# Kernel optimization log

Hardware: AMD Instinct MI355X
Metric: run time of the kernel (lower is better)

The kernel has to match this reference:

```python
import jax, jax.numpy as jnp
import numpy as np

N, T, F, H = 20000, 64, 32, 64
E = 640000
G1, G2 = 64, 32


def _lstm_layer(x_seq, Wih, Whh, bih, bhh):
    # x_seq: [N, T, Fin] -> hs [N, T, H], PyTorch gate order i,f,g,o
    n, _, _ = x_seq.shape
    h_dim = Whh.shape[1]
    h0 = jnp.zeros((n, h_dim), x_seq.dtype)
    c0 = jnp.zeros((n, h_dim), x_seq.dtype)

    def step(carry, xt):
        h, c = carry
        gates = xt @ Wih.T + h @ Whh.T + bih + bhh
        i, f, g, o = jnp.split(gates, 4, axis=-1)
        c = jax.nn.sigmoid(f) * c + jax.nn.sigmoid(i) * jnp.tanh(g)
        h = jax.nn.sigmoid(o) * jnp.tanh(c)
        return (h, c), h

    (_, _), hs = jax.lax.scan(step, (h0, c0), jnp.swapaxes(x_seq, 0, 1))
    return jnp.swapaxes(hs, 0, 1)


def _gcn(h, src, dst, W, b):
    # GCNConv (PyG default): add self-loops, symmetric deg^-1/2 normalization
    n = h.shape[0]
    loop = jnp.arange(n)
    s = jnp.concatenate([src, loop])
    d = jnp.concatenate([dst, loop])
    deg = jax.ops.segment_sum(jnp.ones_like(d, dtype=h.dtype), d, num_segments=n)
    dinv = jnp.where(deg > 0, deg ** -0.5, 0.0)
    norm = dinv[s] * dinv[d]
    xw = h @ W                      # [n, out]
    msg = xw[s] * norm[:, None]     # gather on source nodes
    return jax.ops.segment_sum(msg, d, num_segments=n) + b


def setup_inputs() -> dict:
    key = jax.random.key(0)
    ks = jax.random.split(key, 16)
    s = 0.1
    inp = {
        "x": jax.random.normal(ks[0], (N, T, F), jnp.float32),
        "stock_ids": jax.random.randint(ks[1], (N,), 0, N),
        "edge_index": jax.random.randint(ks[2], (2, E), 0, N),
        # LSTM layer 0
        "Wih0": jax.random.normal(ks[3], (4 * H, F), jnp.float32) * s,
        "Whh0": jax.random.normal(ks[4], (4 * H, H), jnp.float32) * s,
        "bih0": jnp.zeros((4 * H,), jnp.float32),
        "bhh0": jnp.zeros((4 * H,), jnp.float32),
        # LSTM layer 1
        "Wih1": jax.random.normal(ks[5], (4 * H, H), jnp.float32) * s,
        "Whh1": jax.random.normal(ks[6], (4 * H, H), jnp.float32) * s,
        "bih1": jnp.zeros((4 * H,), jnp.float32),
        "bhh1": jnp.zeros((4 * H,), jnp.float32),
        # GCN layers
        "gcn1_W": jax.random.normal(ks[7], (H, G1), jnp.float32) * s,
        "gcn1_b": jnp.zeros((G1,), jnp.float32),
        "gcn2_W": jax.random.normal(ks[8], (G1, G2), jnp.float32) * s,
        "gcn2_b": jnp.zeros((G2,), jnp.float32),
        # head
        "fc_W": jax.random.normal(ks[9], (1, G2), jnp.float32) * s,
        "fc_b": jnp.zeros((1,), jnp.float32),
    }
    return inp


def reference(x, stock_ids, edge_index, Wih0, Whh0, bih0, bhh0,
              Wih1, Whh1, bih1, bhh1, gcn1_W, gcn1_b, gcn2_W, gcn2_b,
              fc_W, fc_b):
    # 2-layer LSTM (eval mode: inter-layer dropout is identity)
    h1 = _lstm_layer(x, Wih0, Whh0, bih0, bhh0)
    h2 = _lstm_layer(h1, Wih1, Whh1, bih1, bhh1)
    h = h2[:, -1, :]                              # [N, H]
    src, dst = edge_index[0], edge_index[1]
    g = jax.nn.relu(_gcn(h, src, dst, gcn1_W, gcn1_b))
    g = jax.nn.relu(_gcn(g, src, dst, gcn2_W, gcn2_b))
    node_features = g[stock_ids]                  # [B, 32]
    out = node_features @ fc_W.T + fc_b           # [B, 1]
    return out.squeeze(-1)
```

## Files before the change

### kernel.cpp

```cpp
#include <hip/hip_runtime.h>
#include <math.h>

#define TT 64
#define FF 32
#define HH 64
#define NN 16
#define GG1 64
#define GG2 32

typedef float f32x4 __attribute__((ext_vector_type(4)));
typedef short bf16x8 __attribute__((ext_vector_type(8)));

__device__ __forceinline__ float fexp2(float x){ return __builtin_amdgcn_exp2f(x); }
__device__ __forceinline__ float frcp (float x){ return __builtin_amdgcn_rcpf(x); }
__device__ __forceinline__ float sigm (float v){ return frcp(1.0f + fexp2(-1.442695041f*v)); }
__device__ __forceinline__ float ftanh(float v){ return fmaf(-2.0f, frcp(1.0f + fexp2(2.885390082f*v)), 1.0f); }

__device__ __forceinline__ float xor8(float v){
  int a = __builtin_bit_cast(int, v);
  int b = __builtin_amdgcn_update_dpp(0, a, 0x128, 0xF, 0xF, true);
  return __builtin_bit_cast(float, b);
}

__device__ __forceinline__ unsigned short bf16rn(float x){
  unsigned u = __builtin_bit_cast(unsigned, x);
  return (unsigned short)((u + 0x7FFFu + ((u >> 16) & 1u)) >> 16);
}
__device__ __forceinline__ void split2(float x, unsigned short& h, unsigned short& l){
  unsigned u = __builtin_bit_cast(unsigned, x);
  unsigned hr = (u + 0x7FFFu + ((u >> 16) & 1u)) & 0xFFFF0000u;
  h = (unsigned short)(hr >> 16);
  l = bf16rn(x - __builtin_bit_cast(float, hr));
}

#define PIN(v) asm volatile("" : "+v"(v))
#define MFMA(acc, a, b) (acc) = __builtin_amdgcn_mfma_f32_16x16x32_bf16((a), (b), (acc), 0, 0, 0)

__device__ __forceinline__ void wsplit(const float* p, bf16x8& hi, bf16x8& lo){
  float4 a = *(const float4*)p;
  float4 b = *(const float4*)(p + 4);
  unsigned short h, s;
  split2(a.x,h,s); hi[0]=(short)h; lo[0]=(short)s;
  split2(a.y,h,s); hi[1]=(short)h; lo[1]=(short)s;
  split2(a.z,h,s); hi[2]=(short)h; lo[2]=(short)s;
  split2(a.w,h,s); hi[3]=(short)h; lo[3]=(short)s;
  split2(b.x,h,s); hi[4]=(short)h; lo[4]=(short)s;
  split2(b.y,h,s); hi[5]=(short)h; lo[5]=(short)s;
  split2(b.z,h,s); hi[6]=(short)h; lo[6]=(short)s;
  split2(b.w,h,s); hi[7]=(short)h; lo[7]=(short)s;
}

__global__ __launch_bounds__(512, 2)
void lstm_mfma(const float* __restrict__ x,
    const float* __restrict__ Wih0, const float* __restrict__ Whh0,
    const float* __restrict__ bih0, const float* __restrict__ bhh0,
    const float* __restrict__ Wih1, const float* __restrict__ Whh1,
    const float* __restrict__ bih1, const float* __restrict__ bhh1,
    float* __restrict__ hout, int n)
{
  const int tid = threadIdx.x;
  const int w   = tid >> 6;
  const int l   = tid & 63;
  const int lr  = l & 15;
  const int lg  = l >> 4;
  const int nA  = blockIdx.x * NN;
  int avail = n - nA; if (avail > NN) avail = NN;

  __shared__ short Ax[2][2][16][40];
  __shared__ short H0[2][2][16][88];
  __shared__ short H1[2][2][16][88];

  const int jm   = lr & 7;
  const int col0 = (lr < 8) ? (8*w + jm) : (64  + 8*w + jm);
  const int col1 = (lr < 8) ? (128 + 8*w + jm) : (192 + 8*w + jm);

  bf16x8 W0h[2][3], W0l[2][3], W1h[2][4], W1l[2][4];
  float bias0[2], bias1[2];
#pragma unroll
  for (int h = 0; h < 2; ++h){
    const int col = h ? col1 : col0;
    wsplit(Wih0 + col*FF + 8*lg,      W0h[h][0], W0l[h][0]);
    wsplit(Whh0 + col*HH + 8*lg,      W0h[h][1], W0l[h][1]);
    wsplit(Whh0 + col*HH + 32 + 8*lg, W0h[h][2], W0l[h][2]);
    wsplit(Wih1 + col*HH + 8*lg,      W1h[h][0], W1l[h][0]);
    wsplit(Wih1 + col*HH + 32 + 8*lg, W1h[h][1], W1l[h][1]);
    wsplit(Whh1 + col*HH + 8*lg,      W1h[h][2], W1l[h][2]);
    wsplit(Whh1 + col*HH + 32 + 8*lg, W1h[h][3], W1l[h][3]);
    bias0[h] = bih0[col] + bhh0[col];
    bias1[h] = bih1[col] + bhh1[col];
  }
#pragma unroll
  for (int h = 0; h < 2; ++h){
#pragma unroll
    for (int k = 0; k < 3; ++k){ PIN(W0h[h][k]); PIN(W0l[h][k]); }
#pragma unroll
    for (int k = 0; k < 4; ++k){ PIN(W1h[h][k]); PIN(W1l[h][k]); }
  }

  {
    short* p0 = &H0[0][0][0][0];
    short* p1 = &H1[0][0][0][0];
    for (int i = tid; i < 2*2*16*88; i += 512){ p0[i] = 0; p1[i] = 0; }
    const int xnd = tid >> 5, xf = tid & 31;
    float v = (xnd < avail) ? x[((size_t)(nA+xnd)*TT + 0)*FF + xf] : 0.0f;
    unsigned short hh, hl; split2(v, hh, hl);
    Ax[0][0][xnd][xf] = (short)hh;
    Ax[0][1][xnd][xf] = (short)hl;
  }
  const int na = 4*lg + ((lr < 8) ? 0 : 2);
  const int nb = na + 1;
  const int m  = 8*w + jm;
  const bool lo8 = (lr < 8);
  float c0a = 0.0f, c0b = 0.0f, c1a = 0.0f, c1b = 0.0f;
  __syncthreads();

  for (int t = 0; t < TT; ++t){
    const int rd0 = (t & 1) ^ 1;
    const int wr0 =  t & 1;
    const int rd1 =  t & 1;
    const int wr1 = (t & 1) ^ 1;

    const int xnd = tid >> 5, xf = tid & 31;
    const int tp = t + 1;
    float xv = 0.0f;
    if (tp < TT && xnd < avail) xv = x[((size_t)(nA+xnd)*TT + tp)*FF + xf];

    bf16x8 axh  = *(const bf16x8*)&Ax[t&1][0][lr][8*lg];
    bf16x8 axl  = *(const bf16x8*)&Ax[t&1][1][lr][8*lg];
    bf16x8 h0ah = *(const bf16x8*)&H0[rd0][0][lr][8*lg];
    bf16x8 h0al = *(const bf16x8*)&H0[rd0][1][lr][8*lg];
    bf16x8 h0bh = *(const bf16x8*)&H0[rd0][0][lr][32+8*lg];
    bf16x8 h0bl = *(const bf16x8*)&H0[rd0][1][lr][32+8*lg];

    f32x4 acc0 = {bias0[0], bias0[0], bias0[0], bias0[0]};
    f32x4 acc1 = {bias0[1], bias0[1], bias0[1], bias0[1]};
    MFMA(acc0, axl,  W0h[0][0]); MFMA(acc0, axh,  W0l[0][0]); MFMA(acc0, axh,  W0h[0][0]);
    MFMA(acc1, axl,  W0h[1][0]); MFMA(acc1, axh,  W0l[1][0]); MFMA(acc1, axh,  W0h[1][0]);
    MFMA(acc0, h0al, W0h[0][1]); MFMA(acc0, h0ah, W0l[0][1]); MFMA(acc0, h0ah, W0h[0][1]);
    MFMA(acc1, h0al, W0h[1][1]); MFMA(acc1, h0ah, W0l[1][1]); MFMA(acc1, h0ah, W0h[1][1]);
    MFMA(acc0, h0bl, W0h[0][2]); MFMA(acc0, h0bh, W0l[0][2]); MFMA(acc0, h0bh, W0h[0][2]);
    MFMA(acc1, h0bl, W0h[1][2]); MFMA(acc1, h0bh, W0l[1][2]); MFMA(acc1, h0bh, W0h[1][2]);

    f32x4 acd0, acd1;
    if (t > 0){
      bf16x8 h1ah = *(const bf16x8*)&H1[rd1][0][lr][8*lg];
      bf16x8 h1al = *(const bf16x8*)&H1[rd1][1][lr][8*lg];
      bf16x8 h1bh = *(const bf16x8*)&H1[rd1][0][lr][32+8*lg];
      bf16x8 h1bl = *(const bf16x8*)&H1[rd1][1][lr][32+8*lg];
      acd0 = (f32x4){bias1[0], bias1[0], bias1[0], bias1[0]};
      acd1 = (f32x4){bias1[1], bias1[1], bias1[1], bias1[1]};
      MFMA(acd0, h0al, W1h[0][0]); MFMA(acd0, h0ah, W1l[0][0]); MFMA(acd0, h0ah, W1h[0][0]);
      MFMA(acd1, h0al, W1h[1][0]); MFMA(acd1, h0ah, W1l[1][0]); MFMA(acd1, h0ah, W1h[1][0]);
      MFMA(acd0, h0bl, W1h[0][1]); MFMA(acd0, h0bh, W1l[0][1]); MFMA(acd0, h0bh, W1h[0][1]);
      MFMA(acd1, h0bl, W1h[1][1]); MFMA(acd1, h0bh, W1l[1][1]); MFMA(acd1, h0bh, W1h[1][1]);
      MFMA(acd0, h1al, W1h[0][2]); MFMA(acd0, h1ah, W1l[0][2]); MFMA(acd0, h1ah, W1h[0][2]);
      MFMA(acd1, h1al, W1h[1][2]); MFMA(acd1, h1ah, W1l[1][2]); MFMA(acd1, h1ah, W1h[1][2]);
      MFMA(acd0, h1bl, W1h[0][3]); MFMA(acd0, h1bh, W1l[0][3]); MFMA(acd0, h1bh, W1h[0][3]);
      MFMA(acd1, h1bl, W1h[1][3]); MFMA(acd1, h1bh, W1l[1][3]); MFMA(acd1, h1bh, W1h[1][3]);
    }

    if (tp < TT){
      unsigned short hh, hl; split2(xv, hh, hl);
      Ax[tp&1][0][xnd][xf] = (short)hh;
      Ax[tp&1][1][xnd][xf] = (short)hl;
    }

    {
      f32x4 s0, s1;
      s0[0]=xor8(acc0[0]); s0[1]=xor8(acc0[1]); s0[2]=xor8(acc0[2]); s0[3]=xor8(acc0[3]);
      s1[0]=xor8(acc1[0]); s1[1]=xor8(acc1[1]); s1[2]=xor8(acc1[2]); s1[3]=xor8(acc1[3]);
      float gi_a = lo8 ? acc0[0] : s0[2],  gi_b = lo8 ? acc0[1] : s0[3];
      float gf_a = lo8 ? s0[0] : acc0[2],  gf_b = lo8 ? s0[1] : acc0[3];
      float gg_a = lo8 ? acc1[0] : s1[2],  gg_b = lo8 ? acc1[1] : s1[3];
      float go_a = lo8 ? s1[0] : acc1[2],  go_b = lo8 ? s1[1] : acc1[3];
      c0a = sigm(gf_a)*c0a + sigm(gi_a)*ftanh(gg_a);
      float ha = sigm(go_a)*ftanh(c0a);
      c0b = sigm(gf_b)*c0b + sigm(gi_b)*ftanh(gg_b);
      float hb = sigm(go_b)*ftanh(c0b);
      unsigned short hh, hl;
      split2(ha, hh, hl); H0[wr0][0][na][m] = (short)hh; H0[wr0][1][na][m] = (short)hl;
      split2(hb, hh, hl); H0[wr0][0][nb][m] = (short)hh; H0[wr0][1][nb][m] = (short)hl;
    }
    if (t > 0){
      f32x4 s0, s1;
      s0[0]=xor8(acd0[0]); s0[1]=xor8(acd0[1]); s0[2]=xor8(acd0[2]); s0[3]=xor8(acd0[3]);
      s1[0]=xor8(acd1[0]); s1[1]=xor8(acd1[1]); s1[2]=xor8(acd1[2]); s1[3]=xor8(acd1[3]);
      float gi_a = lo8 ? acd0[0] : s0[2],  gi_b = lo8 ? acd0[1] : s0[3];
      float gf_a = lo8 ? s0[0] : acd0[2],  gf_b = lo8 ? s0[1] : acd0[3];
      float gg_a = lo8 ? acd1[0] : s1[2],  gg_b = lo8 ? acd1[1] : s1[3];
      float go_a = lo8 ? s1[0] : acd1[2],  go_b = lo8 ? s1[1] : acd1[3];
      c1a = sigm(gf_a)*c1a + sigm(gi_a)*ftanh(gg_a);
      float ha = sigm(go_a)*ftanh(c1a);
      c1b = sigm(gf_b)*c1b + sigm(gi_b)*ftanh(gg_b);
      float hb = sigm(go_b)*ftanh(c1b);
      unsigned short hh, hl;
      split2(ha, hh, hl); H1[wr1][0][na][m] = (short)hh; H1[wr1][1][na][m] = (short)hl;
      split2(hb, hh, hl); H1[wr1][0][nb][m] = (short)hh; H1[wr1][1][nb][m] = (short)hl;
    }
    __syncthreads();
  }

  {
    const int rd0 = (TT-1) & 1;
    const int rd1 =  TT & 1;
    bf16x8 h0ah = *(const bf16x8*)&H0[rd0][0][lr][8*lg];
    bf16x8 h0al = *(const bf16x8*)&H0[rd0][1][lr][8*lg];
    bf16x8 h0bh = *(const bf16x8*)&H0[rd0][0][lr][32+8*lg];
    bf16x8 h0bl = *(const bf16x8*)&H0[rd0][1][lr][32+8*lg];
    bf16x8 h1ah = *(const bf16x8*)&H1[rd1][0][lr][8*lg];
    bf16x8 h1al = *(const bf16x8*)&H1[rd1][1][lr][8*lg];
    bf16x8 h1bh = *(const bf16x8*)&H1[rd1][0][lr][32+8*lg];
    bf16x8 h1bl = *(const bf16x8*)&H1[rd1][1][lr][32+8*lg];
    f32x4 acd0 = {bias1[0], bias1[0], bias1[0], bias1[0]};
    f32x4 acd1 = {bias1[1], bias1[1], bias1[1], bias1[1]};
    MFMA(acd0, h0al, W1h[0][0]); MFMA(acd0, h0ah, W1l[0][0]); MFMA(acd0, h0ah, W1h[0][0]);
    MFMA(acd1, h0al, W1h[1][0]); MFMA(acd1, h0ah, W1l[1][0]); MFMA(acd1, h0ah, W1h[1][0]);
    MFMA(acd0, h0bl, W1h[0][1]); MFMA(acd0, h0bh, W1l[0][1]); MFMA(acd0, h0bh, W1h[0][1]);
    MFMA(acd1, h0bl, W1h[1][1]); MFMA(acd1, h0bh, W1l[1][1]); MFMA(acd1, h0bh, W1h[1][1]);
    MFMA(acd0, h1al, W1h[0][2]); MFMA(acd0, h1ah, W1l[0][2]); MFMA(acd0, h1ah, W1h[0][2]);
    MFMA(acd1, h1al, W1h[1][2]); MFMA(acd1, h1ah, W1l[1][2]); MFMA(acd1, h1ah, W1h[1][2]);
    MFMA(acd0, h1bl, W1h[0][3]); MFMA(acd0, h1bh, W1l[0][3]); MFMA(acd0, h1bh, W1h[0][3]);
    MFMA(acd1, h1bl, W1h[1][3]); MFMA(acd1, h1bh, W1l[1][3]); MFMA(acd1, h1bh, W1h[1][3]);

    f32x4 s0, s1;
    s0[0]=xor8(acd0[0]); s0[1]=xor8(acd0[1]); s0[2]=xor8(acd0[2]); s0[3]=xor8(acd0[3]);
    s1[0]=xor8(acd1[0]); s1[1]=xor8(acd1[1]); s1[2]=xor8(acd1[2]); s1[3]=xor8(acd1[3]);
    float gi_a = lo8 ? acd0[0] : s0[2],  gi_b = lo8 ? acd0[1] : s0[3];
    float gf_a = lo8 ? s0[0] : acd0[2],  gf_b = lo8 ? s0[1] : acd0[3];
    float gg_a = lo8 ? acd1[0] : s1[2],  gg_b = lo8 ? acd1[1] : s1[3];
    float go_a = lo8 ? s1[0] : acd1[2],  go_b = lo8 ? s1[1] : acd1[3];
    c1a = sigm(gf_a)*c1a + sigm(gi_a)*ftanh(gg_a);
    float ha = sigm(go_a)*ftanh(c1a);
    c1b = sigm(gf_b)*c1b + sigm(gi_b)*ftanh(gg_b);
    float hb = sigm(go_b)*ftanh(c1b);
    if (nA + na < n) hout[(size_t)(nA+na)*HH + m] = ha;
    if (nA + nb < n) hout[(size_t)(nA+nb)*HH + m] = hb;
  }
}

__global__ void k_count(const int* __restrict__ dst, int E, int* __restrict__ cnt)
{
  int e = blockIdx.x * blockDim.x + threadIdx.x;
  if (e < E) atomicAdd(&cnt[dst[e]], 1);
}

__global__ void k_scan_build(const int* __restrict__ cnt, int n,
                             int* __restrict__ offs, int* __restrict__ cursor,
                             float* __restrict__ dinv)
{
  __shared__ int part[1024];
  const int tid = threadIdx.x;
  const int per = (n + 1023) >> 10;
  const int base = tid * per;
  int s = 0;
  for (int i = 0; i < per; ++i) { int idx = base + i; if (idx < n) s += cnt[idx]; }
  part[tid] = s;
  __syncthreads();
  for (int off = 1; off < 1024; off <<= 1) {
    int v = 0;
    if (tid >= off) v = part[tid - off];
    __syncthreads();
    part[tid] += v;
    __syncthreads();
  }
  int run = part[tid] - s;
  for (int i = 0; i < per; ++i) {
    int idx = base + i;
    if (idx < n) {
      offs[idx] = run; cursor[idx] = run;
      int c = cnt[idx];
      dinv[idx] = 1.0f / sqrtf((float)(c + 1));
      run += c;
    }
  }
}

__global__ void k_fill(const int* __restrict__ src, const int* __restrict__ dst,
                       int E, int* __restrict__ cursor, int* __restrict__ csr)
{
  int e = blockIdx.x * blockDim.x + threadIdx.x;
  if (e < E) {
    int d = dst[e];
    int pos = atomicAdd(&cursor[d], 1);
    csr[pos] = src[e];
  }
}

template <int K, int M>
__global__ void k_xw(const float* __restrict__ A, const float* __restrict__ W,
                     float* __restrict__ out, int n)
{
  int idx = blockIdx.x * blockDim.x + threadIdx.x;
  int row = idx / M, col = idx % M;
  if (row >= n) return;
  const float* a = A + (size_t)row * K;
  float acc = 0.0f;
#pragma unroll
  for (int k = 0; k < K; ++k) acc = fmaf(a[k], W[k*M + col], acc);
  out[(size_t)row*M + col] = acc;
}

template <int FD>
__global__ void k_agg(const float* __restrict__ xw, const int* __restrict__ offs,
                      const int* __restrict__ cnt, const int* __restrict__ csr,
                      const float* __restrict__ dinv, const float* __restrict__ b,
                      float* __restrict__ out, int n)
{
  int gidx = blockIdx.x * blockDim.x + threadIdx.x;
  int node = gidx / FD, lane = gidx % FD;
  if (node >= n) return;
  const float di = dinv[node];
  float acc = xw[(size_t)node*FD + lane] * di * di;
  const int s0 = offs[node], e0 = s0 + cnt[node];
  for (int p = s0; p < e0; ++p) {
    int s = csr[p];
    acc = fmaf(xw[(size_t)s*FD + lane], dinv[s] * di, acc);
  }
  out[(size_t)node*FD + lane] = fmaxf(acc + b[lane], 0.0f);
}

__global__ void k_fc(const float* __restrict__ g2, const int* __restrict__ sid,
                     const float* __restrict__ fcW, const float* __restrict__ fcb,
                     float* __restrict__ out, int n)
{
  int i = blockIdx.x * blockDim.x + threadIdx.x;
  if (i >= n) return;
  const float* row = g2 + (size_t)sid[i] * GG2;
  float acc = fcb[0];
#pragma unroll
  for (int f = 0; f < GG2; ++f) acc = fmaf(row[f], fcW[f], acc);
  out[i] = acc;
}

extern "C" void kernel_launch(void* const* d_in, const int* in_sizes, int n_in,
                              void* d_out, int out_size, void* d_ws, size_t ws_size,
                              hipStream_t stream)
{
  const float* x    = (const float*)d_in[0];
  const int*   sid  = (const int*)  d_in[1];
  const int*   eidx = (const int*)  d_in[2];
  const float* Wih0 = (const float*)d_in[3];
  const float* Whh0 = (const float*)d_in[4];
  const float* bih0 = (const float*)d_in[5];
  const float* bhh0 = (const float*)d_in[6];
  const float* Wih1 = (const float*)d_in[7];
  const float* Whh1 = (const float*)d_in[8];
  const float* bih1 = (const float*)d_in[9];
  const float* bhh1 = (const float*)d_in[10];
  const float* g1W  = (const float*)d_in[11];
  const float* g1b  = (const float*)d_in[12];
  const float* g2W  = (const float*)d_in[13];
  const float* g2b  = (const float*)d_in[14];
  const float* fcW  = (const float*)d_in[15];
  const float* fcb  = (const float*)d_in[16];

  const int n = in_sizes[1];
  const int E = in_sizes[2] / 2;
  float* out = (float*)d_out;

  char* w = (char*)d_ws;
  auto carve = [&](size_t bytes) -> void* {
    void* p = (void*)w; w += (bytes + 255) & ~(size_t)255; return p;
  };
  float* hfin   = (float*)carve((size_t)n * HH * 4);
  int*   cnt    = (int*)  carve((size_t)n * 4);
  int*   offs   = (int*)  carve((size_t)n * 4);
  int*   cursor = (int*)  carve((size_t)n * 4);
  float* dinv   = (float*)carve((size_t)n * 4);
  int*   csr    = (int*)  carve((size_t)E * 4);
  float* xw1    = (float*)carve((size_t)n * GG1 * 4);
  float* g1     = (float*)carve((size_t)n * GG1 * 4);
  float* xw2    = (float*)carve((size_t)n * GG2 * 4);
  float* g2     = (float*)carve((size_t)n * GG2 * 4);

  const int* src = eidx;
  const int* dst = eidx + E;

  lstm_mfma<<<(n + NN - 1) / NN, 512, 0, stream>>>(x, Wih0, Whh0, bih0, bhh0,
                                                   Wih1, Whh1, bih1, bhh1, hfin, n);

  hipMemsetAsync(cnt, 0, (size_t)n * 4, stream);
  k_count<<<(E + 255) / 256, 256, 0, stream>>>(dst, E, cnt);
  k_scan_build<<<1, 1024, 0, stream>>>(cnt, n, offs, cursor, dinv);
  k_fill<<<(E + 255) / 256, 256, 0, stream>>>(src, dst, E, cursor, csr);

  k_xw<HH, GG1><<<((size_t)n * GG1 + 255) / 256, 256, 0, stream>>>(hfin, g1W, xw1, n);
  k_agg<GG1><<<((size_t)n * GG1 + 255) / 256, 256, 0, stream>>>(xw1, offs, cnt, csr, dinv, g1b, g1, n);

  k_xw<GG1, GG2><<<((size_t)n * GG2 + 255) / 256, 256, 0, stream>>>(g1, g2W, xw2, n);
  k_agg<GG2><<<((size_t)n * GG2 + 255) / 256, 256, 0, stream>>>(xw2, offs, cnt, csr, dinv, g2b, g2, n);

  k_fc<<<(n + 255) / 256, 256, 0, stream>>>(g2, sid, fcW, fcb, out, n);
}
```

Baseline: 692.9 us.

## Split LSTM tile into two node halves and ping-pong MFMA with gate math

Restructures the fused two-layer LSTM loop so the 16-node tile is handled as two 8-row groups. Each group's MFMAs overlap the other group's gate nonlinearities, with two barriers per timestep. Each lane now computes the gates for a single layer (layer 0 or 1, chosen by row), which halves the per-lane transcendental work. It also adds a packed v_cvt_pk_bf16_f32 hi/lo split. In exchange there are twice as many barriers, more live accumulators, and somewhat redundant MFMA work, since each group uses a full 16-row MFMA but only half its rows.

Measured after the change: 945.5 us. 1.36x slower.

```diff
diff --git a/kernel.cpp b/kernel.cpp
--- a/kernel.cpp
+++ b/kernel.cpp
@@ -31,6 +31,13 @@
   unsigned hr = (u + 0x7FFFu + ((u >> 16) & 1u)) & 0xFFFF0000u;
   h = (unsigned short)(hr >> 16);
   l = bf16rn(x - __builtin_bit_cast(float, hr));
+}
+__device__ __forceinline__ void split_pk(float a, float b, unsigned& hi2, unsigned& lo2){
+  asm("v_cvt_pk_bf16_f32 %0, %1, %2" : "=v"(hi2) : "v"(a), "v"(b));
+  float ha = __builtin_bit_cast(float, hi2 << 16);
+  float hb = __builtin_bit_cast(float, hi2 & 0xFFFF0000u);
+  float la = a - ha, lb = b - hb;
+  asm("v_cvt_pk_bf16_f32 %0, %1, %2" : "=v"(lo2) : "v"(la), "v"(lb));
 }
 
 #define PIN(v) asm volatile("" : "+v"(v))
@@ -71,8 +78,9 @@
   __shared__ short H1[2][2][16][88];
 
   const int jm   = lr & 7;
-  const int col0 = (lr < 8) ? (8*w + jm) : (64  + 8*w + jm);
-  const int col1 = (lr < 8) ? (128 + 8*w + jm) : (192 + 8*w + jm);
+  const bool lo8 = (lr < 8);
+  const int col0 = lo8 ? (8*w + jm) : (64  + 8*w + jm);
+  const int col1 = lo8 ? (128 + 8*w + jm) : (192 + 8*w + jm);
 
   bf16x8 W0h[2][3], W0l[2][3], W1h[2][4], W1l[2][4];
   float bias0[2], bias1[2];
@@ -97,6 +105,12 @@
     for (int k = 0; k < 4; ++k){ PIN(W1h[h][k]); PIN(W1l[h][k]); }
   }
 
+  const int na    = 4*lg + (lo8 ? 0 : 2);
+  const int layer = na >> 3;
+  const int rwa   = na & 7;
+  const int rwb   = (na + 1) & 7;
+  const int m     = 8*w + jm;
+
   {
     short* p0 = &H0[0][0][0][0];
     short* p1 = &H1[0][0][0][0];
@@ -107,135 +121,137 @@
     Ax[0][0][xnd][xf] = (short)hh;
     Ax[0][1][xnd][xf] = (short)hl;
   }
-  const int na = 4*lg + ((lr < 8) ? 0 : 2);
-  const int nb = na + 1;
-  const int m  = 8*w + jm;
-  const bool lo8 = (lr < 8);
-  float c0a = 0.0f, c0b = 0.0f, c1a = 0.0f, c1b = 0.0f;
+  float cAa = 0.0f, cAb = 0.0f, cBa = 0.0f, cBb = 0.0f;
+  f32x4 aA0={0,0,0,0}, aA1={0,0,0,0}, dA0={0,0,0,0}, dA1={0,0,0,0};
+  f32x4 aB0={0,0,0,0}, aB1={0,0,0,0}, dB0={0,0,0,0}, dB1={0,0,0,0};
   __syncthreads();
 
-  for (int t = 0; t < TT; ++t){
-    const int rd0 = (t & 1) ^ 1;
-    const int wr0 =  t & 1;
-    const int rd1 =  t & 1;
-    const int wr1 = (t & 1) ^ 1;
-
-    const int xnd = tid >> 5, xf = tid & 31;
-    const int tp = t + 1;
-    float xv = 0.0f;
-    if (tp < TT && xnd < avail) xv = x[((size_t)(nA+xnd)*TT + tp)*FF + xf];
-
-    bf16x8 axh  = *(const bf16x8*)&Ax[t&1][0][lr][8*lg];
-    bf16x8 axl  = *(const bf16x8*)&Ax[t&1][1][lr][8*lg];
-    bf16x8 h0ah = *(const bf16x8*)&H0[rd0][0][lr][8*lg];
-    bf16x8 h0al = *(const bf16x8*)&H0[rd0][1][lr][8*lg];
-    bf16x8 h0bh = *(const bf16x8*)&H0[rd0][0][lr][32+8*lg];
-    bf16x8 h0bl = *(const bf16x8*)&H0[rd0][1][lr][32+8*lg];
-
-    f32x4 acc0 = {bias0[0], bias0[0], bias0[0], bias0[0]};
-    f32x4 acc1 = {bias0[1], bias0[1], bias0[1], bias0[1]};
-    MFMA(acc0, axl,  W0h[0][0]); MFMA(acc0, axh,  W0l[0][0]); MFMA(acc0, axh,  W0h[0][0]);
-    MFMA(acc1, axl,  W0h[1][0]); MFMA(acc1, axh,  W0l[1][0]); MFMA(acc1, axh,  W0h[1][0]);
-    MFMA(acc0, h0al, W0h[0][1]); MFMA(acc0, h0ah, W0l[0][1]); MFMA(acc0, h0ah, W0h[0][1]);
-    MFMA(acc1, h0al, W0h[1][1]); MFMA(acc1, h0ah, W0l[1][1]); MFMA(acc1, h0ah, W0h[1][1]);
-    MFMA(acc0, h0bl, W0h[0][2]); MFMA(acc0, h0bh, W0l[0][2]); MFMA(acc0, h0bh, W0h[0][2]);
-    MFMA(acc1, h0bl, W0h[1][2]); MFMA(acc1, h0bh, W0l[1][2]); MFMA(acc1, h0bh, W0h[1][2]);
-
-    f32x4 acd0, acd1;
-    if (t > 0){
-      bf16x8 h1ah = *(const bf16x8*)&H1[rd1][0][lr][8*lg];
-      bf16x8 h1al = *(const bf16x8*)&H1[rd1][1][lr][8*lg];
-      bf16x8 h1bh = *(const bf16x8*)&H1[rd1][0][lr][32+8*lg];
-      bf16x8 h1bl = *(const bf16x8*)&H1[rd1][1][lr][32+8*lg];
-      acd0 = (f32x4){bias1[0], bias1[0], bias1[0], bias1[0]};
-      acd1 = (f32x4){bias1[1], bias1[1], bias1[1], bias1[1]};
-      MFMA(acd0, h0al, W1h[0][0]); MFMA(acd0, h0ah, W1l[0][0]); MFMA(acd0, h0ah, W1h[0][0]);
-      MFMA(acd1, h0al, W1h[1][0]); MFMA(acd1, h0ah, W1l[1][0]); MFMA(acd1, h0ah, W1h[1][0]);
-      MFMA(acd0, h0bl, W1h[0][1]); MFMA(acd0, h0bh, W1l[0][1]); MFMA(acd0, h0bh, W1h[0][1]);
-      MFMA(acd1, h0bl, W1h[1][1]); MFMA(acd1, h0bh, W1l[1][1]); MFMA(acd1, h0bh, W1h[1][1]);
-      MFMA(acd0, h1al, W1h[0][2]); MFMA(acd0, h1ah, W1l[0][2]); MFMA(acd0, h1ah, W1h[0][2]);
-      MFMA(acd1, h1al, W1h[1][2]); MFMA(acd1, h1ah, W1l[1][2]); MFMA(acd1, h1ah, W1h[1][2]);
-      MFMA(acd0, h1bl, W1h[0][3]); MFMA(acd0, h1bh, W1l[0][3]); MFMA(acd0, h1bh, W1h[0][3]);
-      MFMA(acd1, h1bl, W1h[1][3]); MFMA(acd1, h1bh, W1l[1][3]); MFMA(acd1, h1bh, W1h[1][3]);
-    }
-
+  auto stageX = [&](int tp){
     if (tp < TT){
-      unsigned short hh, hl; split2(xv, hh, hl);
+      const int xnd = tid >> 5, xf = tid & 31;
+      float v = (xnd < avail) ? x[((size_t)(nA+xnd)*TT + tp)*FF + xf] : 0.0f;
+      unsigned short hh, hl; split2(v, hh, hl);
       Ax[tp&1][0][xnd][xf] = (short)hh;
       Ax[tp&1][1][xnd][xf] = (short)hl;
     }
-
-    {
-      f32x4 s0, s1;
-      s0[0]=xor8(acc0[0]); s0[1]=xor8(acc0[1]); s0[2]=xor8(acc0[2]); s0[3]=xor8(acc0[3]);
-      s1[0]=xor8(acc1[0]); s1[1]=xor8(acc1[1]); s1[2]=xor8(acc1[2]); s1[3]=xor8(acc1[3]);
-      float gi_a = lo8 ? acc0[0] : s0[2],  gi_b = lo8 ? acc0[1] : s0[3];
-      float gf_a = lo8 ? s0[0] : acc0[2],  gf_b = lo8 ? s0[1] : acc0[3];
-      float gg_a = lo8 ? acc1[0] : s1[2],  gg_b = lo8 ? acc1[1] : s1[3];
-      float go_a = lo8 ? s1[0] : acc1[2],  go_b = lo8 ? s1[1] : acc1[3];
-      c0a = sigm(gf_a)*c0a + sigm(gi_a)*ftanh(gg_a);
-      float ha = sigm(go_a)*ftanh(c0a);
-      c0b = sigm(gf_b)*c0b + sigm(gi_b)*ftanh(gg_b);
-      float hb = sigm(go_b)*ftanh(c0b);
-      unsigned short hh, hl;
-      split2(ha, hh, hl); H0[wr0][0][na][m] = (short)hh; H0[wr0][1][na][m] = (short)hl;
-      split2(hb, hh, hl); H0[wr0][0][nb][m] = (short)hh; H0[wr0][1][nb][m] = (short)hl;
-    }
-    if (t > 0){
-      f32x4 s0, s1;
-      s0[0]=xor8(acd0[0]); s0[1]=xor8(acd0[1]); s0[2]=xor8(acd0[2]); s0[3]=xor8(acd0[3]);
-      s1[0]=xor8(acd1[0]); s1[1]=xor8(acd1[1]); s1[2]=xor8(acd1[2]); s1[3]=xor8(acd1[3]);
-      float gi_a = lo8 ? acd0[0] : s0[2],  gi_b = lo8 ? acd0[1] : s0[3];
-      float gf_a = lo8 ? s0[0] : acd0[2],  gf_b = lo8 ? s0[1] : acd0[3];
-      float gg_a = lo8 ? acd1[0] : s1[2],  gg_b = lo8 ? acd1[1] : s1[3];
-      float go_a = lo8 ? s1[0] : acd1[2],  go_b = lo8 ? s1[1] : acd1[3];
-      c1a = sigm(gf_a)*c1a + sigm(gi_a)*ftanh(gg_a);
-      float ha = sigm(go_a)*ftanh(c1a);
-      c1b = sigm(gf_b)*c1b + sigm(gi_b)*ftanh(gg_b);
-      float hb = sigm(go_b)*ftanh(c1b);
-      unsigned short hh, hl;
-      split2(ha, hh, hl); H1[wr1][0][na][m] = (short)hh; H1[wr1][1][na][m] = (short)hl;
-      split2(hb, hh, hl); H1[wr1][0][nb][m] = (short)hh; H1[wr1][1][nb][m] = (short)hl;
-    }
+  };
+
+  auto mfmaPh = [&](int g, int bufx, int rd0, int rd1, bool doL0, bool doL1,
+                    f32x4& A0, f32x4& A1, f32x4& D0, f32x4& D1){
+    const int rb = 8*g + (lr & 7);
+    bf16x8 h0ah = *(const bf16x8*)&H0[rd0][0][rb][8*lg];
+    bf16x8 h0al = *(const bf16x8*)&H0[rd0][1][rb][8*lg];
+    bf16x8 h0bh = *(const bf16x8*)&H0[rd0][0][rb][32+8*lg];
+    bf16x8 h0bl = *(const bf16x8*)&H0[rd0][1][rb][32+8*lg];
+    if (doL0){
+      bf16x8 axh = *(const bf16x8*)&Ax[bufx][0][rb][8*lg];
+      bf16x8 axl = *(const bf16x8*)&Ax[bufx][1][rb][8*lg];
+      A0 = (f32x4){bias0[0], bias0[0], bias0[0], bias0[0]};
+      A1 = (f32x4){bias0[1], bias0[1], bias0[1], bias0[1]};
+      MFMA(A0, axl,  W0h[0][0]); MFMA(A0, axh,  W0l[0][0]); MFMA(A0, axh,  W0h[0][0]);
+      MFMA(A1, axl,  W0h[1][0]); MFMA(A1, axh,  W0l[1][0]); MFMA(A1, axh,  W0h[1][0]);
+      MFMA(A0, h0al, W0h[0][1]); MFMA(A0, h0ah, W0l[0][1]); MFMA(A0, h0ah, W0h[0][1]);
+      MFMA(A1, h0al, W0h[1][1]); MFMA(A1, h0ah, W0l[1][1]); MFMA(A1, h0ah, W0h[1][1]);
+      MFMA(A0, h0bl, W0h[0][2]); MFMA(A0, h0bh, W0l[0][2]); MFMA(A0, h0bh, W0h[0][2]);
+      MFMA(A1, h0bl, W0h[1][2]); MFMA(A1, h0bh, W0l[1][2]); MFMA(A1, h0bh, W0h[1][2]);
+    }
+    if (doL1){
+      bf16x8 h1ah = *(const bf16x8*)&H1[rd1][0][rb][8*lg];
+      bf16x8 h1al = *(const bf16x8*)&H1[rd1][1][rb][8*lg];
+      bf16x8 h1bh = *(const bf16x8*)&H1[rd1][0][rb][32+8*lg];
+      bf16x8 h1bl = *(const bf16x8*)&H1[rd1][1][rb][32+8*lg];
+      D0 = (f32x4){bias1[0], bias1[0], bias1[0], bias1[0]};
+      D1 = (f32x4){bias1[1], bias1[1], bias1[1], bias1[1]};
+      MFMA(D0, h0al, W1h[0][0]); MFMA(D0, h0ah, W1l[0][0]); MFMA(D0, h0ah, W1h[0][0]);
+      MFMA(D1, h0al, W1h[1][0]); MFMA(D1, h0ah, W1l[1][0]); MFMA(D1, h0ah, W1h[1][0]);
+      MFMA(D0, h0bl, W1h[0][1]); MFMA(D0, h0bh, W1l[0][1]); MFMA(D0, h0bh, W1h[0][1]);
+      MFMA(D1, h0bl, W1h[1][1]); MFMA(D1, h0bh, W1l[1][1]); MFMA(D1, h0bh, W1h[1][1]);
+      MFMA(D0, h1al, W1h[0][2]); MFMA(D0, h1ah, W1l[0][2]); MFMA(D0, h1ah, W1h[0][2]);
+      MFMA(D1, h1al, W1h[1][2]); MFMA(D1, h1ah, W1l[1][2]); MFMA(D1, h1ah, W1h[1][2]);
+      MFMA(D0, h1bl, W1h[0][3]); MFMA(D0, h1bh, W1l[0][3]); MFMA(D0, h1bh, W1h[0][3]);
+      MFMA(D1, h1bl, W1h[1][3]); MFMA(D1, h1bh, W1l[1][3]); MFMA(D1, h1bh, W1h[1][3]);
+    }
+  };
+
+  auto combinePh = [&](int g, int t, bool doL1,
+                       const f32x4& A0, const f32x4& A1,
+                       const f32x4& D0, const f32x4& D1,
+                       float& ca, float& cb){
+    const int wr0 = t & 1, wr1 = (t & 1) ^ 1;
+    f32x4 P0, P1;
+#pragma unroll
+    for (int i = 0; i < 4; ++i){
+      P0[i] = layer ? D0[i] : A0[i];
+      P1[i] = layer ? D1[i] : A1[i];
+    }
+    f32x4 s0, s1;
+    s0[0]=xor8(P0[0]); s0[1]=xor8(P0[1]); s0[2]=xor8(P0[2]); s0[3]=xor8(P0[3]);
+    s1[0]=xor8(P1[0]); s1[1]=xor8(P1[1]); s1[2]=xor8(P1[2]); s1[3]=xor8(P1[3]);
+    float gi_a = lo8 ? P0[0] : s0[2],  gi_b = lo8 ? P0[1] : s0[3];
+    float gf_a = lo8 ? s0[0] : P0[2],  gf_b = lo8 ? s0[1] : P0[3];
+    float gg_a = lo8 ? P1[0] : s1[2],  gg_b = lo8 ? P1[1] : s1[3];
+    float go_a = lo8 ? s1[0] : P1[2],  go_b = lo8 ? s1[1] : P1[3];
+    if (doL1 || layer == 0){
+      ca = sigm(gf_a)*ca + sigm(gi_a)*ftanh(gg_a);
+      float ha = sigm(go_a)*ftanh(ca);
+      cb = sigm(gf_b)*cb + sigm(gi_b)*ftanh(gg_b);
+      float hb = sigm(go_b)*ftanh(cb);
+      unsigned hi2, lo2; split_pk(ha, hb, hi2, lo2);
+      short* phi = layer ? &H1[wr1][0][0][0] : &H0[wr0][0][0][0];
+      short* plo = layer ? &H1[wr1][1][0][0] : &H0[wr0][1][0][0];
+      const int ra = (8*g + rwa)*88 + m;
+      const int rb = (8*g + rwb)*88 + m;
+      phi[ra] = (short)(hi2 & 0xFFFF);
+      phi[rb] = (short)(hi2 >> 16);
+      plo[ra] = (short)(lo2 & 0xFFFF);
+      plo[rb] = (short)(lo2 >> 16);
+    }
+  };
+
+  auto finalPh = [&](int g, const f32x4& D0, const f32x4& D1, float& ca, float& cb){
+    f32x4 s0, s1;
+    s0[0]=xor8(D0[0]); s0[1]=xor8(D0[1]); s0[2]=xor8(D0[2]); s0[3]=xor8(D0[3]);
+    s1[0]=xor8(D1[0]); s1[1]=xor8(D1[1]); s1[2]=xor8(D1[2]); s1[3]=xor8(D1[3]);
+    float gi_a = lo8 ? D0[0] : s0[2],  gi_b = lo8 ? D0[1] : s0[3];
+    float gf_a = lo8 ? s0[0] : D0[2],  gf_b = lo8 ? s0[1] : D0[3];
+    float gg_a = lo8 ? D1[0] : s1[2],  gg_b = lo8 ? D1[1] : s1[3];
+    float go_a = lo8 ? s1[0] : D1[2],  go_b = lo8 ? s1[1] : D1[3];
+    if (layer == 1){
+      ca = sigm(gf_a)*ca + sigm(gi_a)*ftanh(gg_a);
+      float ha = sigm(go_a)*ftanh(ca);
+      cb = sigm(gf_b)*cb + sigm(gi_b)*ftanh(gg_b);
+      float hb = sigm(go_b)*ftanh(cb);
+      const int node_a = nA + 8*g + rwa;
+      const int node_b = nA + 8*g + rwb;
+      if (node_a < n) hout[(size_t)node_a*HH + m] = ha;
+      if (node_b < n) hout[(size_t)node_b*HH + m] = hb;
+    }
+  };
+
+  mfmaPh(0, 0, 1, 0, true, false, aA0, aA1, dA0, dA1);
+  __syncthreads();
+  mfmaPh(1, 0, 1, 0, true, false, aB0, aB1, dB0, dB1);
+  combinePh(0, 0, false, aA0, aA1, dA0, dA1, cAa, cAb);
+  stageX(1);
+  __syncthreads();
+
+  for (int t = 1; t < TT; ++t){
+    const int bufx = t & 1, rd0 = (t & 1) ^ 1, rd1 = t & 1;
+    mfmaPh(0, bufx, rd0, rd1, true, true, aA0, aA1, dA0, dA1);
+    combinePh(1, t-1, (t-1) > 0, aB0, aB1, dB0, dB1, cBa, cBb);
     __syncthreads();
-  }
-
-  {
-    const int rd0 = (TT-1) & 1;
-    const int rd1 =  TT & 1;
-    bf16x8 h0ah = *(const bf16x8*)&H0[rd0][0][lr][8*lg];
-    bf16x8 h0al = *(const bf16x8*)&H0[rd0][1][lr][8*lg];
-    bf16x8 h0bh = *(const bf16x8*)&H0[rd0][0][lr][32+8*lg];
-    bf16x8 h0bl = *(const bf16x8*)&H0[rd0][1][lr][32+8*lg];
-    bf16x8 h1ah = *(const bf16x8*)&H1[rd1][0][lr][8*lg];
-    bf16x8 h1al = *(const bf16x8*)&H1[rd1][1][lr][8*lg];
-    bf16x8 h1bh = *(const bf16x8*)&H1[rd1][0][lr][32+8*lg];
-    bf16x8 h1bl = *(const bf16x8*)&H1[rd1][1][lr][32+8*lg];
-    f32x4 acd0 = {bias1[0], bias1[0], bias1[0], bias1[0]};
-    f32x4 acd1 = {bias1[1], bias1[1], bias1[1], bias1[1]};
-    MFMA(acd0, h0al, W1h[0][0]); MFMA(acd0, h0ah, W1l[0][0]); MFMA(acd0, h0ah, W1h[0][0]);
-    MFMA(acd1, h0al, W1h[1][0]); MFMA(acd1, h0ah, W1l[1][0]); MFMA(acd1, h0ah, W1h[1][0]);
-    MFMA(acd0, h0bl, W1h[0][1]); MFMA(acd0, h0bh, W1l[0][1]); MFMA(acd0, h0bh, W1h[0][1]);
-    MFMA(acd1, h0bl, W1h[1][1]); MFMA(acd1, h0bh, W1l[1][1]); MFMA(acd1, h0bh, W1h[1][1]);
-    MFMA(acd0, h1al, W1h[0][2]); MFMA(acd0, h1ah, W1l[0][2]); MFMA(acd0, h1ah, W1h[0][2]);
-    MFMA(acd1, h1al, W1h[1][2]); MFMA(acd1, h1ah, W1l[1][2]); MFMA(acd1, h1ah, W1h[1][2]);
-    MFMA(acd0, h1bl, W1h[0][3]); MFMA(acd0, h1bh, W1l[0][3]); MFMA(acd0, h1bh, W1h[0][3]);
-    MFMA(acd1, h1bl, W1h[1][3]); MFMA(acd1, h1bh, W1l[1][3]); MFMA(acd1, h1bh, W1h[1][3]);
-
-    f32x4 s0, s1;
-    s0[0]=xor8(acd0[0]); s0[1]=xor8(acd0[1]); s0[2]=xor8(acd0[2]); s0[3]=xor8(acd0[3]);
-    s1[0]=xor8(acd1[0]); s1[1]=xor8(acd1[1]); s1[2]=xor8(acd1[2]); s1[3]=xor8(acd1[3]);
-    float gi_a = lo8 ? acd0[0] : s0[2],  gi_b = lo8 ? acd0[1] : s0[3];
-    float gf_a = lo8 ? s0[0] : acd0[2],  gf_b = lo8 ? s0[1] : acd0[3];
-    float gg_a = lo8 ? acd1[0] : s1[2],  gg_b = lo8 ? acd1[1] : s1[3];
-    float go_a = lo8 ? s1[0] : acd1[2],  go_b = lo8 ? s1[1] : acd1[3];
-    c1a = sigm(gf_a)*c1a + sigm(gi_a)*ftanh(gg_a);
-    float ha = sigm(go_a)*ftanh(c1a);
-    c1b = sigm(gf_b)*c1b + sigm(gi_b)*ftanh(gg_b);
-    float hb = sigm(go_b)*ftanh(c1b);
-    if (nA + na < n) hout[(size_t)(nA+na)*HH + m] = ha;
-    if (nA + nb < n) hout[(size_t)(nA+nb)*HH + m] = hb;
-  }
+    mfmaPh(1, bufx, rd0, rd1, true, true, aB0, aB1, dB0, dB1);
+    combinePh(0, t, true, aA0, aA1, dA0, dA1, cAa, cAb);
+    stageX(t + 1);
+    __syncthreads();
+  }
+
+  mfmaPh(0, 0, 1, 0, false, true, aA0, aA1, dA0, dA1);
+  combinePh(1, TT-1, true, aB0, aB1, dB0, dB1, cBa, cBb);
+  __syncthreads();
+  mfmaPh(1, 0, 1, 0, false, true, aB0, aB1, dB0, dB1);
+  finalPh(0, dA0, dA1, cAa, cAb);
+  finalPh(1, dB0, dB1, cBa, cBb);
 }
 
 __global__ void k_count(const int* __restrict__ dst, int E, int* __restrict__ cnt)
```

## Split LSTM MFMA accumulator chains and fuse GCN1 aggregation with second XW

Applied to the files above, without the earlier changes.

The input and recurrent contributions in each LSTM gate matmul now go into separate accumulators that are summed afterwards. This splits one long dependent MFMA chain into two independent chains the hardware can interleave, at the cost of extra accumulator registers. Separately, the first GCN aggregation kernel now also computes the second layer's feature transform (g1 @ W2) from shared memory, dropping one kernel launch and a reread of g1. The fused kernel still writes g1 even though nothing appears to read it afterwards.

New measurement: 723.3 us. 4.4% more time.

```diff
diff --git a/kernel.cpp b/kernel.cpp
--- a/kernel.cpp
+++ b/kernel.cpp
@@ -71,8 +71,9 @@
   __shared__ short H1[2][2][16][88];
 
   const int jm   = lr & 7;
-  const int col0 = (lr < 8) ? (8*w + jm) : (64  + 8*w + jm);
-  const int col1 = (lr < 8) ? (128 + 8*w + jm) : (192 + 8*w + jm);
+  const bool lo8 = (lr < 8);
+  const int col0 = lo8 ? (8*w + jm) : (64  + 8*w + jm);
+  const int col1 = lo8 ? (128 + 8*w + jm) : (192 + 8*w + jm);
 
   bf16x8 W0h[2][3], W0l[2][3], W1h[2][4], W1l[2][4];
   float bias0[2], bias1[2];
@@ -107,10 +108,9 @@
     Ax[0][0][xnd][xf] = (short)hh;
     Ax[0][1][xnd][xf] = (short)hl;
   }
-  const int na = 4*lg + ((lr < 8) ? 0 : 2);
+  const int na = 4*lg + (lo8 ? 0 : 2);
   const int nb = na + 1;
   const int m  = 8*w + jm;
-  const bool lo8 = (lr < 8);
   float c0a = 0.0f, c0b = 0.0f, c1a = 0.0f, c1b = 0.0f;
   __syncthreads();
 
@@ -132,31 +132,34 @@
     bf16x8 h0bh = *(const bf16x8*)&H0[rd0][0][lr][32+8*lg];
     bf16x8 h0bl = *(const bf16x8*)&H0[rd0][1][lr][32+8*lg];
 
-    f32x4 acc0 = {bias0[0], bias0[0], bias0[0], bias0[0]};
-    f32x4 acc1 = {bias0[1], bias0[1], bias0[1], bias0[1]};
-    MFMA(acc0, axl,  W0h[0][0]); MFMA(acc0, axh,  W0l[0][0]); MFMA(acc0, axh,  W0h[0][0]);
-    MFMA(acc1, axl,  W0h[1][0]); MFMA(acc1, axh,  W0l[1][0]); MFMA(acc1, axh,  W0h[1][0]);
-    MFMA(acc0, h0al, W0h[0][1]); MFMA(acc0, h0ah, W0l[0][1]); MFMA(acc0, h0ah, W0h[0][1]);
-    MFMA(acc1, h0al, W0h[1][1]); MFMA(acc1, h0ah, W0l[1][1]); MFMA(acc1, h0ah, W0h[1][1]);
-    MFMA(acc0, h0bl, W0h[0][2]); MFMA(acc0, h0bh, W0l[0][2]); MFMA(acc0, h0bh, W0h[0][2]);
-    MFMA(acc1, h0bl, W0h[1][2]); MFMA(acc1, h0bh, W0l[1][2]); MFMA(acc1, h0bh, W0h[1][2]);
-
-    f32x4 acd0, acd1;
+    f32x4 ax0 = {bias0[0], bias0[0], bias0[0], bias0[0]};
+    f32x4 ax1 = {bias0[1], bias0[1], bias0[1], bias0[1]};
+    f32x4 ah0 = {0.f,0.f,0.f,0.f}, ah1 = {0.f,0.f,0.f,0.f};
+    MFMA(ax0, axl,  W0h[0][0]); MFMA(ax0, axh,  W0l[0][0]); MFMA(ax0, axh,  W0h[0][0]);
+    MFMA(ax1, axl,  W0h[1][0]); MFMA(ax1, axh,  W0l[1][0]); MFMA(ax1, axh,  W0h[1][0]);
+    MFMA(ah0, h0al, W0h[0][1]); MFMA(ah0, h0ah, W0l[0][1]); MFMA(ah0, h0ah, W0h[0][1]);
+    MFMA(ah1, h0al, W0h[1][1]); MFMA(ah1, h0ah, W0l[1][1]); MFMA(ah1, h0ah, W0h[1][1]);
+    MFMA(ah0, h0bl, W0h[0][2]); MFMA(ah0, h0bh, W0l[0][2]); MFMA(ah0, h0bh, W0h[0][2]);
+    MFMA(ah1, h0bl, W0h[1][2]); MFMA(ah1, h0bh, W0l[1][2]); MFMA(ah1, h0bh, W0h[1][2]);
+
+    f32x4 ap0, ap1, aq0, aq1;
     if (t > 0){
       bf16x8 h1ah = *(const bf16x8*)&H1[rd1][0][lr][8*lg];
       bf16x8 h1al = *(const bf16x8*)&H1[rd1][1][lr][8*lg];
       bf16x8 h1bh = *(const bf16x8*)&H1[rd1][0][lr][32+8*lg];
       bf16x8 h1bl = *(const bf16x8*)&H1[rd1][1][lr][32+8*lg];
-      acd0 = (f32x4){bias1[0], bias1[0], bias1[0], bias1[0]};
-      acd1 = (f32x4){bias1[1], bias1[1], bias1[1], bias1[1]};
-      MFMA(acd0, h0al, W1h[0][0]); MFMA(acd0, h0ah, W1l[0][0]); MFMA(acd0, h0ah, W1h[0][0]);
-      MFMA(acd1, h0al, W1h[1][0]); MFMA(acd1, h0ah, W1l[1][0]); MFMA(acd1, h0ah, W1h[1][0]);
-      MFMA(acd0, h0bl, W1h[0][1]); MFMA(acd0, h0bh, W1l[0][1]); MFMA(acd0, h0bh, W1h[0][1]);
-      MFMA(acd1, h0bl, W1h[1][1]); MFMA(acd1, h0bh, W1l[1][1]); MFMA(acd1, h0bh, W1h[1][1]);
-      MFMA(acd0, h1al, W1h[0][2]); MFMA(acd0, h1ah, W1l[0][2]); MFMA(acd0, h1ah, W1h[0][2]);
-      MFMA(acd1, h1al, W1h[1][2]); MFMA(acd1, h1ah, W1l[1][2]); MFMA(acd1, h1ah, W1h[1][2]);
-      MFMA(acd0, h1bl, W1h[0][3]); MFMA(acd0, h1bh, W1l[0][3]); MFMA(acd0, h1bh, W1h[0][3]);
-      MFMA(acd1, h1bl, W1h[1][3]); MFMA(acd1, h1bh, W1l[1][3]); MFMA(acd1, h1bh, W1h[1][3]);
+      ap0 = (f32x4){bias1[0], bias1[0], bias1[0], bias1[0]};
+      ap1 = (f32x4){bias1[1], bias1[1], bias1[1], bias1[1]};
+      aq0 = (f32x4){0.f,0.f,0.f,0.f};
+      aq1 = (f32x4){0.f,0.f,0.f,0.f};
+      MFMA(ap0, h0al, W1h[0][0]); MFMA(ap0, h0ah, W1l[0][0]); MFMA(ap0, h0ah, W1h[0][0]);
+      MFMA(ap1, h0al, W1h[1][0]); MFMA(ap1, h0ah, W1l[1][0]); MFMA(ap1, h0ah, W1h[1][0]);
+      MFMA(ap0, h0bl, W1h[0][1]); MFMA(ap0, h0bh, W1l[0][1]); MFMA(ap0, h0bh, W1h[0][1]);
+      MFMA(ap1, h0bl, W1h[1][1]); MFMA(ap1, h0bh, W1l[1][1]); MFMA(ap1, h0bh, W1h[1][1]);
+      MFMA(aq0, h1al, W1h[0][2]); MFMA(aq0, h1ah, W1l[0][2]); MFMA(aq0, h1ah, W1h[0][2]);
+      MFMA(aq1, h1al, W1h[1][2]); MFMA(aq1, h1ah, W1l[1][2]); MFMA(aq1, h1ah, W1h[1][2]);
+      MFMA(aq0, h1bl, W1h[0][3]); MFMA(aq0, h1bh, W1l[0][3]); MFMA(aq0, h1bh, W1h[0][3]);
+      MFMA(aq1, h1bl, W1h[1][3]); MFMA(aq1, h1bh, W1l[1][3]); MFMA(aq1, h1bh, W1h[1][3]);
     }
 
     if (tp < TT){
@@ -166,6 +169,8 @@
     }
 
     {
+      f32x4 acc0 = ax0 + ah0;
+      f32x4 acc1 = ax1 + ah1;
       f32x4 s0, s1;
       s0[0]=xor8(acc0[0]); s0[1]=xor8(acc0[1]); s0[2]=xor8(acc0[2]); s0[3]=xor8(acc0[3]);
       s1[0]=xor8(acc1[0]); s1[1]=xor8(acc1[1]); s1[2]=xor8(acc1[2]); s1[3]=xor8(acc1[3]);
@@ -182,6 +187,8 @@
       split2(hb, hh, hl); H0[wr0][0][nb][m] = (short)hh; H0[wr0][1][nb][m] = (short)hl;
     }
     if (t > 0){
+      f32x4 acd0 = ap0 + aq0;
+      f32x4 acd1 = ap1 + aq1;
       f32x4 s0, s1;
       s0[0]=xor8(acd0[0]); s0[1]=xor8(acd0[1]); s0[2]=xor8(acd0[2]); s0[3]=xor8(acd0[3]);
       s1[0]=xor8(acd1[0]); s1[1]=xor8(acd1[1]); s1[2]=xor8(acd1[2]); s1[3]=xor8(acd1[3]);
@@ -211,17 +218,20 @@
     bf16x8 h1al = *(const bf16x8*)&H1[rd1][1][lr][8*lg];
     bf16x8 h1bh = *(const bf16x8*)&H1[rd1][0][lr][32+8*lg];
     bf16x8 h1bl = *(const bf16x8*)&H1[rd1][1][lr][32+8*lg];
-    f32x4 acd0 = {bias1[0], bias1[0], bias1[0], bias1[0]};
-    f32x4 acd1 = {bias1[1], bias1[1], bias1[1], bias1[1]};
-    MFMA(acd0, h0al, W1h[0][0]); MFMA(acd0, h0ah, W1l[0][0]); MFMA(acd0, h0ah, W1h[0][0]);
-    MFMA(acd1, h0al, W1h[1][0]); MFMA(acd1, h0ah, W1l[1][0]); MFMA(acd1, h0ah, W1h[1][0]);
-    MFMA(acd0, h0bl, W1h[0][1]); MFMA(acd0, h0bh, W1l[0][1]); MFMA(acd0, h0bh, W1h[0][1]);
-    MFMA(acd1, h0bl, W1h[1][1]); MFMA(acd1, h0bh, W1l[1][1]); MFMA(acd1, h0bh, W1h[1][1]);
-    MFMA(acd0, h1al, W1h[0][2]); MFMA(acd0, h1ah, W1l[0][2]); MFMA(acd0, h1ah, W1h[0][2]);
-    MFMA(acd1, h1al, W1h[1][2]); MFMA(acd1, h1ah, W1l[1][2]); MFMA(acd1, h1ah, W1h[1][2]);
-    MFMA(acd0, h1bl, W1h[0][3]); MFMA(acd0, h1bh, W1l[0][3]); MFMA(acd0, h1bh, W1h[0][3]);
-    MFMA(acd1, h1bl, W1h[1][3]); MFMA(acd1, h1bh, W1l[1][3]); MFMA(acd1, h1bh, W1h[1][3]);
-
+    f32x4 ap0 = {bias1[0], bias1[0], bias1[0], bias1[0]};
+    f32x4 ap1 = {bias1[1], bias1[1], bias1[1], bias1[1]};
+    f32x4 aq0 = {0.f,0.f,0.f,0.f}, aq1 = {0.f,0.f,0.f,0.f};
+    MFMA(ap0, h0al, W1h[0][0]); MFMA(ap0, h0ah, W1l[0][0]); MFMA(ap0, h0ah, W1h[0][0]);
+    MFMA(ap1, h0al, W1h[1][0]); MFMA(ap1, h0ah, W1l[1][0]); MFMA(ap1, h0ah, W1h[1][0]);
+    MFMA(ap0, h0bl, W1h[0][1]); MFMA(ap0, h0bh, W1l[0][1]); MFMA(ap0, h0bh, W1h[0][1]);
+    MFMA(ap1, h0bl, W1h[1][1]); MFMA(ap1, h0bh, W1l[1][1]); MFMA(ap1, h0bh, W1h[1][1]);
+    MFMA(aq0, h1al, W1h[0][2]); MFMA(aq0, h1ah, W1l[0][2]); MFMA(aq0, h1ah, W1h[0][2]);
+    MFMA(aq1, h1al, W1h[1][2]); MFMA(aq1, h1ah, W1l[1][2]); MFMA(aq1, h1ah, W1h[1][2]);
+    MFMA(aq0, h1bl, W1h[0][3]); MFMA(aq0, h1bh, W1l[0][3]); MFMA(aq0, h1bh, W1h[0][3]);
+    MFMA(aq1, h1bl, W1h[1][3]); MFMA(aq1, h1bh, W1l[1][3]); MFMA(aq1, h1bh, W1h[1][3]);
+
+    f32x4 acd0 = ap0 + aq0;
+    f32x4 acd1 = ap1 + aq1;
     f32x4 s0, s1;
     s0[0]=xor8(acd0[0]); s0[1]=xor8(acd0[1]); s0[2]=xor8(acd0[2]); s0[3]=xor8(acd0[3]);
     s1[0]=xor8(acd1[0]); s1[1]=xor8(acd1[1]); s1[2]=xor8(acd1[2]); s1[3]=xor8(acd1[3]);
@@ -298,6 +308,37 @@
 #pragma unroll
   for (int k = 0; k < K; ++k) acc = fmaf(a[k], W[k*M + col], acc);
   out[(size_t)row*M + col] = acc;
+}
+
+__global__ void k_agg_x2(const float* __restrict__ xw, const int* __restrict__ offs,
+                         const int* __restrict__ cnt, const int* __restrict__ csr,
+                         const float* __restrict__ dinv, const float* __restrict__ b,
+                         const float* __restrict__ W2,
+                         float* __restrict__ g1out, float* __restrict__ xw2out, int n)
+{
+  __shared__ float sg[4][GG1];
+  const int nd   = threadIdx.x >> 6;
+  const int lane = threadIdx.x & 63;
+  const int node = blockIdx.x * 4 + nd;
+  if (node < n) {
+    const float di = dinv[node];
+    float acc = xw[(size_t)node*GG1 + lane] * di * di;
+    const int s0 = offs[node], e0 = s0 + cnt[node];
+    for (int p = s0; p < e0; ++p) {
+      int s = csr[p];
+      acc = fmaf(xw[(size_t)s*GG1 + lane], dinv[s] * di, acc);
+    }
+    float val = fmaxf(acc + b[lane], 0.0f);
+    g1out[(size_t)node*GG1 + lane] = val;
+    sg[nd][lane] = val;
+  }
+  __syncthreads();
+  if (node < n && lane < GG2) {
+    float a2 = 0.0f;
+#pragma unroll
+    for (int k = 0; k < GG1; ++k) a2 = fmaf(sg[nd][k], W2[k*GG2 + lane], a2);
+    xw2out[(size_t)node*GG2 + lane] = a2;
+  }
 }
 
 template <int FD>
@@ -385,9 +426,8 @@
   k_fill<<<(E + 255) / 256, 256, 0, stream>>>(src, dst, E, cursor, csr);
 
   k_xw<HH, GG1><<<((size_t)n * GG1 + 255) / 256, 256, 0, stream>>>(hfin, g1W, xw1, n);
-  k_agg<GG1><<<((size_t)n * GG1 + 255) / 256, 256, 0, stream>>>(xw1, offs, cnt, csr, dinv, g1b, g1, n);
-
-  k_xw<GG1, GG2><<<((size_t)n * GG2 + 255) / 256, 256, 0, stream>>>(g1, g2W, xw2, n);
+  k_agg_x2<<<(n + 3) / 4, 256, 0, stream>>>(xw1, offs, cnt, csr, dinv, g1b, g2W, g1, xw2, n);
+
   k_agg<GG2><<<((size_t)n * GG2 + 255) / 256, 256, 0, stream>>>(xw2, offs, cnt, csr, dinv, g2b, g2, n);
 
   k_fc<<<(n + 255) / 256, 256, 0, stream>>>(g2, sid, fcW, fcb, out, n);
```
